# Optimization experiments

Measured on AMD Instinct MI355X. Metric: run time of the kernel, lower is better.

Reference implementation:

```python
import jax, jax.numpy as jnp
import numpy as np

GRAPH = 50  # top-k neighbors


def setup_inputs() -> dict:
    key = jax.random.key(0)
    k1, k2, k3, k4, k5 = jax.random.split(key, 5)
    B, N, D, C = 2048, 50000, 256, 100
    return {
        "features": jax.random.normal(k1, (B, D), dtype=jnp.float32),
        "anchor_feature": jax.random.normal(k2, (N, D), dtype=jnp.float32),
        "labels": jax.random.randint(k3, (B,), 0, C),
        "t_labels": jax.random.randint(k4, (B,), 0, C),
        "anchor_label": jax.random.randint(k5, (N,), 0, C),
    }


def reference(features, anchor_feature, labels, t_labels, anchor_label):
    # mode == 'knn_sim', reduction=False; t_labels is unpacked but unused.
    # [B, N] dot-product similarity
    sim = jnp.matmul(features, anchor_feature.T)
    # top-k values and indices along anchor dim
    topk_vals, topk_idx = jax.lax.top_k(sim, GRAPH)  # [B, k]
    # label-match mask gathered at the top-k anchors (equivalent to
    # building the full [B, N] eq-mask then torch.gather along dim 1,
    # but gathers anchor labels first to avoid the dense mask)
    nn_labels = anchor_label[topk_idx]               # [B, k]
    mask_k = (labels[:, None] == nn_labels).astype(jnp.float32)
    mean_log_prob_pos = mask_k.sum(axis=1) / GRAPH   # [B]
    mean_sim = topk_vals.sum(axis=1) / GRAPH         # [B]
    # NaN scrub (x != x) -> 0, as in the torch code
    mean_log_prob_pos = jnp.where(jnp.isnan(mean_log_prob_pos), 0.0, mean_log_prob_pos)
    loss = -mean_log_prob_pos                        # [B] (reduction=False)
    return loss, mean_sim
```

## Files before the change

### kernel.cpp

```cpp
#include <hip/hip_runtime.h>
#include <math.h>

#define B_ROWS 2048
#define N_ANCH 50000
#define DIM    256
#define TOPK   50

#define BTS 128
#define BTL 256
#define AT 256
#define KC 32
#define NCHUNK 8
#define NCH 16
#define CHUNK 3125
#define NTILES 13
#define NSAMP 4096
#define CAPG 2048

#define TSF  (16 * 8 * 512)
#define TSF2 (8 * 8 * 1024)
#define TSA  (NCH * NTILES * 8 * 1024)

typedef __attribute__((ext_vector_type(8))) short bf16x8;
typedef __attribute__((ext_vector_type(8))) unsigned short u16x8;
typedef __attribute__((ext_vector_type(4))) float f32x4;

#define OFF_A_S 16384
#define BUFB_S  24576
#define OFF_A_L 16384
#define BUFB_L  32768

__device__ __forceinline__ void gl_lds16(const void* g, void* l) {
    __builtin_amdgcn_global_load_lds(
        (const __attribute__((address_space(1))) unsigned int*)g,
        (__attribute__((address_space(3))) unsigned int*)l, 16, 0, 0);
}

template<int N>
__device__ __forceinline__ void wait_vmcnt() {
    asm volatile("s_waitcnt vmcnt(%0)" :: "n"(N) : "memory");
}
__device__ __forceinline__ void wait_lgkm0() {
    asm volatile("s_waitcnt lgkmcnt(0)" ::: "memory");
}
__device__ __forceinline__ void pipe_bar() {
    asm volatile("" ::: "memory");
    __builtin_amdgcn_s_barrier();
    asm volatile("" ::: "memory");
}

__device__ __forceinline__ unsigned short f2bf(float x) {
    unsigned u = __float_as_uint(x);
    u += 0x7FFFu + ((u >> 16) & 1u);
    return (unsigned short)(u >> 16);
}

__device__ __forceinline__ unsigned f2ord(float f) {
    unsigned u = __float_as_uint(f);
    return (u & 0x80000000u) ? ~u : (u | 0x80000000u);
}
__device__ __forceinline__ float ord2f(unsigned o) {
    return (o & 0x80000000u) ? __uint_as_float(o & 0x7FFFFFFFu) : __uint_as_float(~o);
}

__device__ __forceinline__ void cvt8(const float4 v0, const float4 v1,
                                     u16x8* H, u16x8* L) {
    float f[8] = {v0.x, v0.y, v0.z, v0.w, v1.x, v1.y, v1.z, v1.w};
    u16x8 h, l;
    #pragma unroll
    for (int j = 0; j < 8; ++j) {
        unsigned short hb = f2bf(f[j]);
        h[j] = hb;
        l[j] = f2bf(f[j] - __uint_as_float((unsigned)hb << 16));
    }
    *H = h; *L = l;
}

__global__ __launch_bounds__(256)
void split_pack_feat(const float* __restrict__ x,
                     unsigned short* __restrict__ hi,
                     unsigned short* __restrict__ lo)
{
    const int S  = blockIdx.x * 256 + threadIdx.x;
    const int s  = S & 511;
    const int c  = (S >> 9) & 7;
    const int rb = S >> 12;
    const int r  = s & 127;
    const int kq = s >> 7;
    const int row = (rb << 7) + r;
    const int k   = (c << 5) + (kq << 3);
    const float4* src = (const float4*)(x + (size_t)row * DIM + k);
    u16x8 H, L;
    cvt8(src[0], src[1], &H, &L);
    *(u16x8*)(hi + (size_t)S * 8) = H;
    *(u16x8*)(lo + (size_t)S * 8) = L;
}

__global__ __launch_bounds__(256)
void split_pack_feat256(const float* __restrict__ x,
                        unsigned short* __restrict__ hi,
                        unsigned short* __restrict__ lo)
{
    const int S  = blockIdx.x * 256 + threadIdx.x;
    const int s  = S & 1023;
    const int c  = (S >> 10) & 7;
    const int rb = S >> 13;
    const int r  = s & 255;
    const int kq = s >> 8;
    const int row = (rb << 8) + r;
    const int k   = (c << 5) + (kq << 3);
    const float4* src = (const float4*)(x + (size_t)row * DIM + k);
    u16x8 H, L;
    cvt8(src[0], src[1], &H, &L);
    *(u16x8*)(hi + (size_t)S * 8) = H;
    *(u16x8*)(lo + (size_t)S * 8) = L;
}

__global__ __launch_bounds__(256)
void split_pack_anc(const float* __restrict__ x,
                    unsigned short* __restrict__ hi,
                    unsigned short* __restrict__ lo)
{
    const int S    = blockIdx.x * 256 + threadIdx.x;
    const int s    = S & 1023;
    const int c    = (S >> 10) & 7;
    const int tg   = S >> 13;
    const int cidx = tg / NTILES;
    const int tile = tg - cidx * NTILES;
    int a = cidx * CHUNK + (tile << 8) + (s & 255);
    if (a >= N_ANCH) a = N_ANCH - 1;
    const int k = (c << 5) + ((s >> 8) << 3);
    const float4* src = (const float4*)(x + (size_t)a * DIM + k);
    u16x8 H, L;
    cvt8(src[0], src[1], &H, &L);
    *(u16x8*)(hi + (size_t)S * 8) = H;
    *(u16x8*)(lo + (size_t)S * 8) = L;
}


#define STAGE_LOADS_S 3
__device__ __forceinline__ void stage_tile_s(unsigned char* sb,
                                             const unsigned short* __restrict__ Bsrc,
                                             const unsigned short* __restrict__ Asrc,
                                             int w, int lane)
{
    #pragma unroll
    for (int i = 0; i < 2; ++i) {
        const int t = (w << 1) + i;
        gl_lds16(Bsrc + ((size_t)t << 9) + (lane << 3), sb + (t << 10));
    }
    gl_lds16(Asrc + (((w << 6) + lane) << 3), sb + OFF_A_S + (w << 10));
}

__device__ __forceinline__ void compute_tile_s(const unsigned char* sb,
                                               int wm, int wn, int quad, int lx,
                                               f32x4 (&acc)[4][4])
{
    bf16x8 bf[4], af[4];
    #pragma unroll
    for (int tn = 0; tn < 4; ++tn) {
        const int a = (wn << 6) + (tn << 4) + lx;
        bf[tn] = *(const bf16x8*)(sb + (quad << 12) + (a << 4));
    }
    #pragma unroll
    for (int tm = 0; tm < 4; ++tm) {
        const int r = (wm << 6) + (tm << 4) + lx;
        af[tm] = *(const bf16x8*)(sb + OFF_A_S + (quad << 11) + (r << 4));
    }
    #pragma unroll
    for (int tm = 0; tm < 4; ++tm)
        #pragma unroll
        for (int tn = 0; tn < 4; ++tn)
            acc[tm][tn] = __builtin_amdgcn_mfma_f32_16x16x32_bf16(af[tm], bf[tn], acc[tm][tn], 0, 0, 0);
}

__global__ __launch_bounds__(512, 4)
void knn_sample_gemm(const unsigned short* __restrict__ pfhi,
                     const unsigned short* __restrict__ pflo,
                     const unsigned short* __restrict__ pahi,
                     const unsigned short* __restrict__ palo,
                     float* __restrict__ sims)
{
    __shared__ __align__(16) unsigned char sMem[2 * BUFB_S];

    const int tid  = threadIdx.x;
    const int w    = tid >> 6;
    const int lane = tid & 63;
    const int quad = lane >> 4;
    const int lx   = lane & 15;
    const int wm   = w >> 2;
    const int wn   = w & 3;

    const int id   = blockIdx.x;
    const int xcd  = id & 7;
    const int t    = id >> 3;
    const int rb   = t & 15;
    const int cidx = ((t >> 4) << 3) | xcd;
    const int rbase = rb * BTS;
    const int tg    = cidx * NTILES;

    const unsigned short* Fp[3] = {pfhi, pflo, pfhi};
    const unsigned short* Bp[3] = {pahi, pahi, palo};

    auto bsrc = [&](int it) {
        return Bp[it >> 3] + (((size_t)(tg << 3)) + (it & 7)) * 8192;
    };
    auto asrc = [&](int it) {
        return Fp[it >> 3] + (((size_t)(rb << 3)) + (it & 7)) * 4096;
    };

    f32x4 acc[4][4];
    const f32x4 z = {0.f, 0.f, 0.f, 0.f};
    #pragma unroll
    for (int tm = 0; tm < 4; ++tm)
        #pragma unroll
        for (int tn = 0; tn < 4; ++tn) acc[tm][tn] = z;

    stage_tile_s(sMem, bsrc(0), asrc(0), w, lane);
    __syncthreads();

    int cur = 0;
    for (int it = 0; it < 24; ++it) {
        if (it + 1 < 24) {
            stage_tile_s(sMem + (cur ^ 1) * BUFB_S, bsrc(it + 1), asrc(it + 1), w, lane);
            wait_vmcnt<STAGE_LOADS_S>();
        } else {
            wait_vmcnt<0>();
        }
        pipe_bar();
        compute_tile_s(sMem + cur * BUFB_S, wm, wn, quad, lx, acc);
        wait_lgkm0();
        pipe_bar();
        cur ^= 1;
    }

    #pragma unroll
    for (int tm = 0; tm < 4; ++tm)
        #pragma unroll
        for (int tn = 0; tn < 4; ++tn)
            #pragma unroll
            for (int reg = 0; reg < 4; ++reg) {
                int row = rbase + (wm << 6) + (tm << 4) + (quad << 2) + reg;
                int col = (wn << 6) + (tn << 4) + lx;
                sims[(size_t)row * NSAMP + cidx * AT + col] = acc[tm][tn][reg];
            }
}

__global__ __launch_bounds__(256)
void bisect_thresh(const float* __restrict__ sims,
                   uint2* __restrict__ cand, int* __restrict__ cnt,
                   float* __restrict__ Tarr)
{
    __shared__ float sv[NSAMP];
    __shared__ float s_rmin[4], s_rmax[4];
    __shared__ int   s_c, s_ns;

    const int row = blockIdx.x;
    const int tid = threadIdx.x;
    const int lane = tid & 63, w = tid >> 6;
    const unsigned long long below = (lane == 0) ? 0ull : (~0ull >> (64 - lane));

    const float4* S4 = (const float4*)(sims + (size_t)row * NSAMP);
    for (int i = tid; i < NSAMP / 4; i += 256) ((float4*)sv)[i] = S4[i];
    __syncthreads();

    float lmin = INFINITY, lmax = -INFINITY;
    for (int e0 = 0; e0 < NSAMP; e0 += 256) {
        float v = sv[e0 + tid];
        lmin = fminf(lmin, v); lmax = fmaxf(lmax, v);
    }
    #pragma unroll
    for (int off = 32; off; off >>= 1) {
        lmin = fminf(lmin, __shfl_down(lmin, off));
        lmax = fmaxf(lmax, __shfl_down(lmax, off));
    }
    if (lane == 0) { s_rmin[w] = lmin; s_rmax[w] = lmax; }
    __syncthreads();
    float lo = fminf(fminf(s_rmin[0], s_rmin[1]), fminf(s_rmin[2], s_rmin[3]));
    float mx = fmaxf(fmaxf(s_rmax[0], s_rmax[1]), fmaxf(s_rmax[2], s_rmax[3]));
    float hi = ord2f(f2ord(mx) + 1);
    int clo = NSAMP;
    for (int it = 0; it < 32 && clo > 64; ++it) {
        float mid = 0.5f * (lo + hi);
        if (tid == 0) s_c = 0;
        __syncthreads();
        int lc = 0;
        for (int e0 = 0; e0 < NSAMP; e0 += 256) lc += (sv[e0 + tid] >= mid);
        #pragma unroll
        for (int off = 32; off; off >>= 1) lc += __shfl_down(lc, off);
        if (lane == 0) atomicAdd(&s_c, lc);
        __syncthreads();
        int c = s_c;
        if (c >= TOPK) { lo = mid; clo = c; } else hi = mid;
        __syncthreads();
    }
    if (tid == 0) { Tarr[row] = lo; s_ns = 0; }
    __syncthreads();

    for (int e0 = 0; e0 < NSAMP; e0 += 256) {
        int e = e0 + tid;
        float v = sv[e];
        bool pred = (v >= lo);
        unsigned long long mk = __ballot(pred);
        int base = 0;
        if (lane == 0) base = atomicAdd(&s_ns, __popcll(mk));
        base = __shfl(base, 0);
        if (pred) {
            int ofs = base + __popcll(mk & below);
            int anchor = (e >> 8) * CHUNK + (e & 255);
            cand[(size_t)row * CAPG + ofs] = make_uint2(__float_as_uint(v), (unsigned)anchor);
        }
    }
    __syncthreads();
    if (tid == 0) cnt[row] = s_ns;
}


#define STAGE_LOADS_L 2
__device__ __forceinline__ void stage_tile_l(unsigned char* sb,
                                             const unsigned short* __restrict__ Bsrc,
                                             const unsigned short* __restrict__ Asrc,
                                             int w, int lane)
{
    gl_lds16(Bsrc + ((size_t)w << 9) + (lane << 3), sb + (w << 10));
    gl_lds16(Asrc + ((size_t)w << 9) + (lane << 3), sb + OFF_A_L + (w << 10));
}

__device__ __forceinline__ void compute_tile_l(const unsigned char* sb,
                                               int wm, int wn, int quad, int lx,
                                               f32x4 (&acc)[4][4])
{
    bf16x8 bf[4], af[4];
    #pragma unroll
    for (int tn = 0; tn < 4; ++tn) {
        const int a = (wn << 6) + (tn << 4) + lx;
        bf[tn] = *(const bf16x8*)(sb + (quad << 12) + (a << 4));
    }
    #pragma unroll
    for (int tm = 0; tm < 4; ++tm) {
        const int r = (wm << 6) + (tm << 4) + lx;
        af[tm] = *(const bf16x8*)(sb + OFF_A_L + (quad << 12) + (r << 4));
    }
    #pragma unroll
    for (int tm = 0; tm < 4; ++tm)
        #pragma unroll
        for (int tn = 0; tn < 4; ++tn)
            acc[tm][tn] = __builtin_amdgcn_mfma_f32_16x16x32_bf16(af[tm], bf[tn], acc[tm][tn], 0, 0, 0);
}

__global__ __launch_bounds__(1024, 4)
void knn_mfma_append(const unsigned short* __restrict__ qfhi,
                     const unsigned short* __restrict__ qflo,
                     const unsigned short* __restrict__ pahi,
                     const unsigned short* __restrict__ palo,
                     const float* __restrict__ Tarr,
                     uint2* __restrict__ cand, int* __restrict__ cnt)
{
    __shared__ __align__(16) unsigned char sMem[2 * BUFB_L];
    __shared__ float s_T[BTL];

    const int tid  = threadIdx.x;
    const int w    = tid >> 6;
    const int lane = tid & 63;
    const int quad = lane >> 4;
    const int lx   = lane & 15;
    const int wm   = w >> 2;
    const int wn   = w & 3;

    const int id   = blockIdx.x;
    const int xcd  = id & 7;
    const int t    = id >> 3;
    const int rb   = t & 7;
    const int gseq = t >> 3;
    const int g    = (gseq << 3) | xcd;
    const int cidx = g & 15;
    const int tile = 1 + (g >> 4);
    const int rbase = rb * BTL;

    if (tid < BTL) s_T[tid] = Tarr[rbase + tid];

    const unsigned short* Fp[3] = {qfhi, qflo, qfhi};
    const unsigned short* Bp[3] = {pahi, pahi, palo};

    auto bsrc = [&](int it) {
        return Bp[it >> 3] + (((size_t)((cidx * NTILES + tile) << 3)) + (it & 7)) * 8192;
    };
    auto asrc = [&](int it) {
        return Fp[it >> 3] + (((size_t)(rb << 3)) + (it & 7)) * 8192;
    };

    stage_tile_l(sMem, bsrc(0), asrc(0), w, lane);
    __syncthreads();

    float thr[4][4];
    #pragma unroll
    for (int tm = 0; tm < 4; ++tm)
        #pragma unroll
        for (int reg = 0; reg < 4; ++reg)
            thr[tm][reg] = s_T[(wm << 6) + (tm << 4) + (quad << 2) + reg];

    f32x4 acc[4][4];
    const f32x4 z = {0.f, 0.f, 0.f, 0.f};
    #pragma unroll
    for (int tm = 0; tm < 4; ++tm)
        #pragma unroll
        for (int tn = 0; tn < 4; ++tn) acc[tm][tn] = z;

    int cur = 0;
    for (int it = 0; it < 24; ++it) {
        if (it + 1 < 24) {
            stage_tile_l(sMem + (cur ^ 1) * BUFB_L, bsrc(it + 1), asrc(it + 1), w, lane);
            wait_vmcnt<STAGE_LOADS_L>();
        } else {
            wait_vmcnt<0>();
        }
        pipe_bar();
        compute_tile_l(sMem + cur * BUFB_L, wm, wn, quad, lx, acc);
        wait_lgkm0();
        pipe_bar();
        cur ^= 1;
    }

    const int abase = cidx * CHUNK + tile * AT;
    const int valid = min(AT, CHUNK - tile * AT);

    #pragma unroll
    for (int tm = 0; tm < 4; ++tm)
        #pragma unroll
        for (int tn = 0; tn < 4; ++tn)
            #pragma unroll
            for (int reg = 0; reg < 4; ++reg) {
                const float v    = acc[tm][tn][reg];
                const int   aoff = (wn << 6) + (tn << 4) + lx;
                if (aoff < valid && v >= thr[tm][reg]) {
                    const int row = rbase + (wm << 6) + (tm << 4) + (quad << 2) + reg;
                    int slot = atomicAdd(&cnt[row], 1);
                    if (slot < CAPG)
                        cand[(size_t)row * CAPG + slot] =
                            make_uint2(__float_as_uint(v), (unsigned)(abase + aoff));
                }
            }
}

__global__ __launch_bounds__(256)
void knn_final(const uint2* __restrict__ cand, const int* __restrict__ cnt,
               const int* __restrict__ labels, const int* __restrict__ anchor_label,
               float* __restrict__ out)
{
    __shared__ float pv[CAPG];
    __shared__ int   pi[CAPG];
    __shared__ float fv[128];
    __shared__ int   fi[128];
    __shared__ float s_rmin[4], s_rmax[4];
    __shared__ int   s_c, s_m, s_cm;
    __shared__ float s_sum;

    const int row = blockIdx.x;
    const int tid = threadIdx.x;
    const int lane = tid & 63, w = tid >> 6;
    const unsigned long long below = (lane == 0) ? 0ull : (~0ull >> (64 - lane));

    if (tid == 0) { s_sum = 0.f; s_cm = 0; }

    int ns = cnt[row]; if (ns > CAPG) ns = CAPG;
    for (int e0 = 0; e0 < ns; e0 += 256) {
        int e = e0 + tid;
        if (e < ns) {
            uint2 c = cand[(size_t)row * CAPG + e];
            pv[e] = __uint_as_float(c.x); pi[e] = (int)c.y;
        }
    }
    __syncthreads();
    const int mylab = labels[row];

    float lmin = INFINITY, lmax = -INFINITY;
    for (int e0 = 0; e0 < ns; e0 += 256) {
        int e = e0 + tid;
        if (e < ns) { float v = pv[e]; lmin = fminf(lmin, v); lmax = fmaxf(lmax, v); }
    }
    #pragma unroll
    for (int off = 32; off; off >>= 1) {
        lmin = fminf(lmin, __shfl_down(lmin, off));
        lmax = fmaxf(lmax, __shfl_down(lmax, off));
    }
    if (lane == 0) { s_rmin[w] = lmin; s_rmax[w] = lmax; }
    __syncthreads();
    float lo = fminf(fminf(s_rmin[0], s_rmin[1]), fminf(s_rmin[2], s_rmin[3]));
    float mx = fmaxf(fmaxf(s_rmax[0], s_rmax[1]), fmaxf(s_rmax[2], s_rmax[3]));
    float hi = ord2f(f2ord(mx) + 1);
    int clo = ns;
    for (int it = 0; it < 32 && clo > 96; ++it) {
        float mid = 0.5f * (lo + hi);
        if (tid == 0) s_c = 0;
        __syncthreads();
        int lc = 0;
        for (int e0 = 0; e0 < ns; e0 += 256) {
            int e = e0 + tid;
            lc += (e < ns && pv[e] >= mid);
        }
        #pragma unroll
        for (int off = 32; off; off >>= 1) lc += __shfl_down(lc, off);
        if (lane == 0) atomicAdd(&s_c, lc);
        __syncthreads();
        int c = s_c;
        if (c >= TOPK) { lo = mid; clo = c; } else hi = mid;
        __syncthreads();
    }

    if (clo <= 96) {
        if (tid == 0) s_m = 0;
        __syncthreads();
        for (int e0 = 0; e0 < ns; e0 += 256) {
            int e = e0 + tid;
            bool pred = (e < ns) && (pv[e] >= lo);
            unsigned long long mk = __ballot(pred);
            int base = 0;
            if (lane == 0) base = atomicAdd(&s_m, __popcll(mk));
            base = __shfl(base, 0);
            if (pred) {
                int ofs = base + __popcll(mk & below);
                fv[ofs] = pv[e]; fi[ofs] = pi[e];
            }
        }
        __syncthreads();
        const int m = s_m;
        if (tid < m) {
            float v = fv[tid]; int id = fi[tid];
            int r = 0;
            for (int q = 0; q < m; ++q) {
                float vq = fv[q];
                r += (vq > v) || (vq == v && fi[q] < id);
            }
            if (r < TOPK) {
                atomicAdd(&s_sum, v);
                if (anchor_label[id] == mylab) atomicAdd(&s_cm, 1);
            }
        }
    } else {
        for (int e0 = 0; e0 < ns; e0 += 256) {
            int e = e0 + tid;
            if (e < ns) {
                float v = pv[e]; int id = pi[e];
                int r = 0;
                for (int q = 0; q < ns; ++q) {
                    float vq = pv[q];
                    r += (vq > v) || (vq == v && pi[q] < id);
                }
                if (r < TOPK) {
                    atomicAdd(&s_sum, v);
                    if (anchor_label[id] == mylab) atomicAdd(&s_cm, 1);
                }
            }
        }
    }
    __syncthreads();
    if (tid == 0) {
        float mlp = (float)s_cm / (float)TOPK;
        out[row]          = -mlp;
        out[B_ROWS + row] = s_sum / (float)TOPK;
    }
}

extern "C" void kernel_launch(void* const* d_in, const int* in_sizes, int n_in,
                              void* d_out, int out_size, void* d_ws, size_t ws_size,
                              hipStream_t stream)
{
    const float* feat         = (const float*)d_in[0];
    const float* anc          = (const float*)d_in[1];
    const int*   labels       = (const int*)d_in[2];
    const int*   anchor_label = (const int*)d_in[4];
    float* out = (float*)d_out;

    char* ws = (char*)d_ws;
    size_t off = 0;
    unsigned short* pfhi = (unsigned short*)(ws + off); off += (size_t)TSF * 16;
    unsigned short* pflo = (unsigned short*)(ws + off); off += (size_t)TSF * 16;
    unsigned short* qfhi = (unsigned short*)(ws + off); off += (size_t)TSF2 * 16;
    unsigned short* qflo = (unsigned short*)(ws + off); off += (size_t)TSF2 * 16;
    unsigned short* pahi = (unsigned short*)(ws + off); off += (size_t)TSA * 16;
    unsigned short* palo = (unsigned short*)(ws + off); off += (size_t)TSA * 16;
    float* sims = (float*)(ws + off);        off += (size_t)B_ROWS * NSAMP * 4;
    uint2* cand = (uint2*)sims;
    int*   cnt  = (int*)(ws + off);          off += (size_t)B_ROWS * 4;
    float* Tarr = (float*)(ws + off);        off += (size_t)B_ROWS * 4;

    hipLaunchKernelGGL(split_pack_feat, dim3(TSF / 256), dim3(256), 0, stream,
                       feat, pfhi, pflo);
    hipLaunchKernelGGL(split_pack_feat256, dim3(TSF2 / 256), dim3(256), 0, stream,
                       feat, qfhi, qflo);
    hipLaunchKernelGGL(split_pack_anc, dim3(TSA / 256), dim3(256), 0, stream,
                       anc, pahi, palo);
    hipLaunchKernelGGL(knn_sample_gemm, dim3(256), dim3(512), 0, stream,
                       pfhi, pflo, pahi, palo, sims);
    hipLaunchKernelGGL(bisect_thresh, dim3(B_ROWS), dim3(256), 0, stream,
                       sims, cand, cnt, Tarr);
    hipLaunchKernelGGL(knn_mfma_append, dim3(1536), dim3(1024), 0, stream,
                       qfhi, qflo, pahi, palo, Tarr, cand, cnt);
    hipLaunchKernelGGL(knn_final, dim3(B_ROWS), dim3(256), 0, stream,
                       cand, cnt, labels, anchor_label, out);
}
```

Measured before the change: 558.0 us.

## Fuse split-bf16 passes per K chunk and triple-buffer sample GEMM

The main append GEMM now stages the hi and lo parts of both operands for one K chunk together and issues all three split-precision MFMA products (hi*hi, lo*hi, hi*lo) from that single stage. Before, it ran 24 separate passes over the same data. This means 8 pipeline iterations instead of 24, with fewer barriers, and the hi fragments are reused across products. The sample GEMM moves to a 3-stage LDS ring with prefetch depth two and one barrier per iteration, and s_setprio brackets around the MFMA blocks. The cost is 128KB of LDS per block in the append kernel, which can lower occupancy, and the threshold loads now happen after the loop.

```diff
diff --git a/kernel.cpp b/kernel.cpp
--- a/kernel.cpp
+++ b/kernel.cpp
@@ -25,10 +25,16 @@
 typedef __attribute__((ext_vector_type(8))) unsigned short u16x8;
 typedef __attribute__((ext_vector_type(4))) float f32x4;
 
-#define OFF_A_S 16384
-#define BUFB_S  24576
-#define OFF_A_L 16384
-#define BUFB_L  32768
+#define OFF_B 0
+#define OFF_A 16384
+#define BUFB  24576
+#define SMEM_S (3 * BUFB)
+
+#define OFF_BH 0
+#define OFF_BL 16384
+#define OFF_AH 32768
+#define OFF_AL 49152
+#define BUFF   65536
 
 __device__ __forceinline__ void gl_lds16(const void* g, void* l) {
     __builtin_amdgcn_global_load_lds(
@@ -138,40 +144,42 @@
 }
 
 
-#define STAGE_LOADS_S 3
-__device__ __forceinline__ void stage_tile_s(unsigned char* sb,
-                                             const unsigned short* __restrict__ Bsrc,
-                                             const unsigned short* __restrict__ Asrc,
-                                             int w, int lane)
+#define STAGE_LOADS 3
+__device__ __forceinline__ void stage_tile(unsigned char* sb,
+                                           const unsigned short* __restrict__ Bsrc,
+                                           const unsigned short* __restrict__ Asrc,
+                                           int w, int lane)
 {
     #pragma unroll
     for (int i = 0; i < 2; ++i) {
         const int t = (w << 1) + i;
-        gl_lds16(Bsrc + ((size_t)t << 9) + (lane << 3), sb + (t << 10));
-    }
-    gl_lds16(Asrc + (((w << 6) + lane) << 3), sb + OFF_A_S + (w << 10));
-}
-
-__device__ __forceinline__ void compute_tile_s(const unsigned char* sb,
-                                               int wm, int wn, int quad, int lx,
-                                               f32x4 (&acc)[4][4])
+        gl_lds16(Bsrc + ((size_t)t << 9) + (lane << 3), sb + OFF_B + (t << 10));
+    }
+    gl_lds16(Asrc + (((w << 6) + lane) << 3), sb + OFF_A + (w << 10));
+}
+
+__device__ __forceinline__ void compute_tile(const unsigned char* sb,
+                                             int wm, int wn, int quad, int lx,
+                                             f32x4 (&acc)[4][4])
 {
     bf16x8 bf[4], af[4];
     #pragma unroll
     for (int tn = 0; tn < 4; ++tn) {
         const int a = (wn << 6) + (tn << 4) + lx;
-        bf[tn] = *(const bf16x8*)(sb + (quad << 12) + (a << 4));
+        bf[tn] = *(const bf16x8*)(sb + OFF_B + (quad << 12) + (a << 4));
     }
     #pragma unroll
     for (int tm = 0; tm < 4; ++tm) {
         const int r = (wm << 6) + (tm << 4) + lx;
-        af[tm] = *(const bf16x8*)(sb + OFF_A_S + (quad << 11) + (r << 4));
-    }
+        af[tm] = *(const bf16x8*)(sb + OFF_A + (quad << 11) + (r << 4));
+    }
+    __builtin_amdgcn_s_setprio(1);
     #pragma unroll
     for (int tm = 0; tm < 4; ++tm)
         #pragma unroll
         for (int tn = 0; tn < 4; ++tn)
             acc[tm][tn] = __builtin_amdgcn_mfma_f32_16x16x32_bf16(af[tm], bf[tn], acc[tm][tn], 0, 0, 0);
+    __builtin_amdgcn_s_setprio(0);
 }
 
 __global__ __launch_bounds__(512, 4)
@@ -181,7 +189,7 @@
                      const unsigned short* __restrict__ palo,
                      float* __restrict__ sims)
 {
-    __shared__ __align__(16) unsigned char sMem[2 * BUFB_S];
+    __shared__ __align__(16) unsigned char sMem[SMEM_S];
 
     const int tid  = threadIdx.x;
     const int w    = tid >> 6;
@@ -216,22 +224,18 @@
         #pragma unroll
         for (int tn = 0; tn < 4; ++tn) acc[tm][tn] = z;
 
-    stage_tile_s(sMem, bsrc(0), asrc(0), w, lane);
-    __syncthreads();
-
-    int cur = 0;
+    stage_tile(sMem + 0 * BUFB, bsrc(0), asrc(0), w, lane);
+    stage_tile(sMem + 1 * BUFB, bsrc(1), asrc(1), w, lane);
+    __syncthreads();
+
     for (int it = 0; it < 24; ++it) {
-        if (it + 1 < 24) {
-            stage_tile_s(sMem + (cur ^ 1) * BUFB_S, bsrc(it + 1), asrc(it + 1), w, lane);
-            wait_vmcnt<STAGE_LOADS_S>();
-        } else {
-            wait_vmcnt<0>();
-        }
+        if (it + 2 < 24)
+            stage_tile(sMem + ((it + 2) % 3) * BUFB, bsrc(it + 2), asrc(it + 2), w, lane);
+        compute_tile(sMem + (it % 3) * BUFB, wm, wn, quad, lx, acc);
+        wait_lgkm0();
+        if (it + 2 < 24)      wait_vmcnt<STAGE_LOADS>();
+        else if (it + 1 < 24) wait_vmcnt<0>();
         pipe_bar();
-        compute_tile_s(sMem + cur * BUFB_S, wm, wn, quad, lx, acc);
-        wait_lgkm0();
-        pipe_bar();
-        cur ^= 1;
     }
 
     #pragma unroll
@@ -316,36 +320,69 @@
 }
 
 
-#define STAGE_LOADS_L 2
-__device__ __forceinline__ void stage_tile_l(unsigned char* sb,
-                                             const unsigned short* __restrict__ Bsrc,
-                                             const unsigned short* __restrict__ Asrc,
-                                             int w, int lane)
-{
-    gl_lds16(Bsrc + ((size_t)w << 9) + (lane << 3), sb + (w << 10));
-    gl_lds16(Asrc + ((size_t)w << 9) + (lane << 3), sb + OFF_A_L + (w << 10));
-}
-
-__device__ __forceinline__ void compute_tile_l(const unsigned char* sb,
-                                               int wm, int wn, int quad, int lx,
-                                               f32x4 (&acc)[4][4])
-{
-    bf16x8 bf[4], af[4];
+#define STAGE_LOADS_F 4
+__device__ __forceinline__ void stage_fused(unsigned char* sb,
+                                            const unsigned short* __restrict__ Bh,
+                                            const unsigned short* __restrict__ Bl,
+                                            const unsigned short* __restrict__ Ah,
+                                            const unsigned short* __restrict__ Al,
+                                            int w, int lane)
+{
+    const int o = ((w << 6) + lane) << 3;
+    gl_lds16(Bh + o, sb + OFF_BH + (w << 10));
+    gl_lds16(Bl + o, sb + OFF_BL + (w << 10));
+    gl_lds16(Ah + o, sb + OFF_AH + (w << 10));
+    gl_lds16(Al + o, sb + OFF_AL + (w << 10));
+}
+
+__device__ __forceinline__ void compute_fused(const unsigned char* sb,
+                                              int wm, int wn, int quad, int lx,
+                                              f32x4 (&acc)[4][4])
+{
+    bf16x8 afh[4], bfh[4], afl[4], bfl[4];
     #pragma unroll
     for (int tn = 0; tn < 4; ++tn) {
         const int a = (wn << 6) + (tn << 4) + lx;
-        bf[tn] = *(const bf16x8*)(sb + (quad << 12) + (a << 4));
+        bfh[tn] = *(const bf16x8*)(sb + OFF_BH + (quad << 12) + (a << 4));
     }
     #pragma unroll
     for (int tm = 0; tm < 4; ++tm) {
         const int r = (wm << 6) + (tm << 4) + lx;
-        af[tm] = *(const bf16x8*)(sb + OFF_A_L + (quad << 12) + (r << 4));
-    }
+        afh[tm] = *(const bf16x8*)(sb + OFF_AH + (quad << 12) + (r << 4));
+    }
+    __builtin_amdgcn_s_setprio(1);
     #pragma unroll
     for (int tm = 0; tm < 4; ++tm)
         #pragma unroll
         for (int tn = 0; tn < 4; ++tn)
-            acc[tm][tn] = __builtin_amdgcn_mfma_f32_16x16x32_bf16(af[tm], bf[tn], acc[tm][tn], 0, 0, 0);
+            acc[tm][tn] = __builtin_amdgcn_mfma_f32_16x16x32_bf16(afh[tm], bfh[tn], acc[tm][tn], 0, 0, 0);
+    __builtin_amdgcn_s_setprio(0);
+
+    #pragma unroll
+    for (int tm = 0; tm < 4; ++tm) {
+        const int r = (wm << 6) + (tm << 4) + lx;
+        afl[tm] = *(const bf16x8*)(sb + OFF_AL + (quad << 12) + (r << 4));
+    }
+    __builtin_amdgcn_s_setprio(1);
+    #pragma unroll
+    for (int tm = 0; tm < 4; ++tm)
+        #pragma unroll
+        for (int tn = 0; tn < 4; ++tn)
+            acc[tm][tn] = __builtin_amdgcn_mfma_f32_16x16x32_bf16(afl[tm], bfh[tn], acc[tm][tn], 0, 0, 0);
+    __builtin_amdgcn_s_setprio(0);
+
+    #pragma unroll
+    for (int tn = 0; tn < 4; ++tn) {
+        const int a = (wn << 6) + (tn << 4) + lx;
+        bfl[tn] = *(const bf16x8*)(sb + OFF_BL + (quad << 12) + (a << 4));
+    }
+    __builtin_amdgcn_s_setprio(1);
+    #pragma unroll
+    for (int tm = 0; tm < 4; ++tm)
+        #pragma unroll
+        for (int tn = 0; tn < 4; ++tn)
+            acc[tm][tn] = __builtin_amdgcn_mfma_f32_16x16x32_bf16(afh[tm], bfl[tn], acc[tm][tn], 0, 0, 0);
+    __builtin_amdgcn_s_setprio(0);
 }
 
 __global__ __launch_bounds__(1024, 4)
@@ -356,7 +393,7 @@
                      const float* __restrict__ Tarr,
                      uint2* __restrict__ cand, int* __restrict__ cnt)
 {
-    __shared__ __align__(16) unsigned char sMem[2 * BUFB_L];
+    __shared__ __align__(16) unsigned char sMem[2 * BUFF];
     __shared__ float s_T[BTL];
 
     const int tid  = threadIdx.x;
@@ -379,25 +416,10 @@
 
     if (tid < BTL) s_T[tid] = Tarr[rbase + tid];
 
-    const unsigned short* Fp[3] = {qfhi, qflo, qfhi};
-    const unsigned short* Bp[3] = {pahi, pahi, palo};
-
-    auto bsrc = [&](int it) {
-        return Bp[it >> 3] + (((size_t)((cidx * NTILES + tile) << 3)) + (it & 7)) * 8192;
-    };
-    auto asrc = [&](int it) {
-        return Fp[it >> 3] + (((size_t)(rb << 3)) + (it & 7)) * 8192;
-    };
-
-    stage_tile_l(sMem, bsrc(0), asrc(0), w, lane);
-    __syncthreads();
-
-    float thr[4][4];
-    #pragma unroll
-    for (int tm = 0; tm < 4; ++tm)
-        #pragma unroll
-        for (int reg = 0; reg < 4; ++reg)
-            thr[tm][reg] = s_T[(wm << 6) + (tm << 4) + (quad << 2) + reg];
+    const unsigned short* Bh0 = pahi + ((size_t)(cidx * NTILES + tile) << 3) * 8192;
+    const unsigned short* Bl0 = palo + ((size_t)(cidx * NTILES + tile) << 3) * 8192;
+    const unsigned short* Ah0 = qfhi + ((size_t)rb << 3) * 8192;
+    const unsigned short* Al0 = qflo + ((size_t)rb << 3) * 8192;
 
     f32x4 acc[4][4];
     const f32x4 z = {0.f, 0.f, 0.f, 0.f};
@@ -406,20 +428,31 @@
         #pragma unroll
         for (int tn = 0; tn < 4; ++tn) acc[tm][tn] = z;
 
-    int cur = 0;
-    for (int it = 0; it < 24; ++it) {
-        if (it + 1 < 24) {
-            stage_tile_l(sMem + (cur ^ 1) * BUFB_L, bsrc(it + 1), asrc(it + 1), w, lane);
-            wait_vmcnt<STAGE_LOADS_L>();
+    stage_fused(sMem, Bh0, Bl0, Ah0, Al0, w, lane);
+    __syncthreads();
+
+    for (int c = 0; c < NCHUNK; ++c) {
+        if (c + 1 < NCHUNK) {
+            stage_fused(sMem + ((c + 1) & 1) * BUFF,
+                        Bh0 + (size_t)(c + 1) * 8192, Bl0 + (size_t)(c + 1) * 8192,
+                        Ah0 + (size_t)(c + 1) * 8192, Al0 + (size_t)(c + 1) * 8192,
+                        w, lane);
+            wait_vmcnt<STAGE_LOADS_F>();
         } else {
             wait_vmcnt<0>();
         }
         pipe_bar();
-        compute_tile_l(sMem + cur * BUFB_L, wm, wn, quad, lx, acc);
+        compute_fused(sMem + (c & 1) * BUFF, wm, wn, quad, lx, acc);
         wait_lgkm0();
         pipe_bar();
-        cur ^= 1;
-    }
+    }
+
+    float thr[4][4];
+    #pragma unroll
+    for (int tm = 0; tm < 4; ++tm)
+        #pragma unroll
+        for (int reg = 0; reg < 4; ++reg)
+            thr[tm][reg] = s_T[(wm << 6) + (tm << 4) + (quad << 2) + reg];
 
     const int abase = cidx * CHUNK + tile * AT;
     const int valid = min(AT, CHUNK - tile * AT);
```

Measured after the change: 528.3 us, median of 3. -5.3%, faster.
